# Kernel tuning notes

Hardware: AMD Instinct MI355X
Metric: run time of the kernel (lower is better)

## Reference

```python
import jax, jax.numpy as jnp
import numpy as np

B, N, S, D, H = 32, 16384, 8, 64, 128  # batch, num_inputs, num_slots, slot_size(==input_size), mlp_hidden
ITERS = 3
EPS = 1e-8
LN_EPS = 1e-5


def _ln(x, g, b):
    m = jnp.mean(x, axis=-1, keepdims=True)
    v = jnp.mean((x - m) ** 2, axis=-1, keepdims=True)
    return (x - m) * jax.lax.rsqrt(v + LN_EPS) * g + b


def setup_inputs() -> dict:
    key = jax.random.key(0)
    ks = jax.random.split(key, 20)
    s = 0.02
    return {
        "x": jax.random.normal(ks[0], (B, N, D), jnp.float32),
        "slot_noise": jax.random.normal(ks[1], (B, S, D), jnp.float32),
        "slots_mu": jax.random.normal(ks[2], (1, S, D), jnp.float32),
        "slots_log_sigma": jax.random.normal(ks[3], (1, S, D), jnp.float32) * 0.1,
        "ln_in_g": jnp.ones((D,), jnp.float32), "ln_in_b": jnp.zeros((D,), jnp.float32),
        "ln_slot_g": jnp.ones((D,), jnp.float32), "ln_slot_b": jnp.zeros((D,), jnp.float32),
        "ln_mlp_g": jnp.ones((D,), jnp.float32), "ln_mlp_b": jnp.zeros((D,), jnp.float32),
        "Wq": jax.random.normal(ks[4], (D, D), jnp.float32) * s,
        "Wk": jax.random.normal(ks[5], (D, D), jnp.float32) * s,
        "Wv": jax.random.normal(ks[6], (D, D), jnp.float32) * s,
        "W_ih": jax.random.normal(ks[7], (3 * D, D), jnp.float32) * s,
        "W_hh": jax.random.normal(ks[8], (3 * D, D), jnp.float32) * s,
        "b_ih": jnp.zeros((3 * D,), jnp.float32),
        "b_hh": jnp.zeros((3 * D,), jnp.float32),
        "W1": jax.random.normal(ks[9], (H, D), jnp.float32) * s,
        "b1": jnp.zeros((H,), jnp.float32),
        "W2": jax.random.normal(ks[10], (D, H), jnp.float32) * s,
        "b2": jnp.zeros((D,), jnp.float32),
    }


def reference(x, slot_noise, slots_mu, slots_log_sigma,
              ln_in_g, ln_in_b, ln_slot_g, ln_slot_b, ln_mlp_g, ln_mlp_b,
              Wq, Wk, Wv, W_ih, W_hh, b_ih, b_hh, W1, b1, W2, b2):
    inputs = _ln(x, ln_in_g, ln_in_b)                      # [B,N,D]
    keys = inputs @ Wk.T                                   # [B,N,D]
    values = inputs @ Wv.T                                 # [B,N,D]
    slots = slots_mu + jnp.exp(slots_log_sigma) * slot_noise  # [B,S,D]
    scale = D ** (-0.5)
    for _ in range(ITERS):
        slots_prev = slots
        q = (_ln(slots, ln_slot_g, ln_slot_b) @ Wq.T) * scale   # [B,S,D]
        attn = jax.nn.softmax(jnp.einsum('bnd,bsd->bns', keys, q), axis=2) + EPS
        attn = attn / jnp.sum(attn, axis=1, keepdims=True)      # weighted mean over inputs
        updates = jnp.einsum('bns,bnd->bsd', attn, values)      # [B,S,D]
        # GRUCell(update, hidden=slots_prev), torch semantics
        gi = updates @ W_ih.T + b_ih
        gh = slots_prev @ W_hh.T + b_hh
        i_r, i_z, i_n = jnp.split(gi, 3, axis=-1)
        h_r, h_z, h_n = jnp.split(gh, 3, axis=-1)
        r = jax.nn.sigmoid(i_r + h_r)
        z = jax.nn.sigmoid(i_z + h_z)
        n = jnp.tanh(i_n + r * h_n)
        upd = (1.0 - z) * n + z * slots_prev
        # residual MLP (full_skip=False: residual around updates)
        slots = upd + jax.nn.relu(_ln(upd, ln_mlp_g, ln_mlp_b) @ W1.T + b1) @ W2.T + b2
    return slots
```

## Files before the change

kernel.cpp:

```cpp
#include <hip/hip_runtime.h>

#define BB 32
#define NN 16384

typedef __attribute__((ext_vector_type(4))) float f4;
typedef __attribute__((ext_vector_type(8))) short short8;

__device__ __forceinline__ unsigned int f2bf(float f) {
  unsigned int u = __float_as_uint(f);
  return (u + 0x7fffu + ((u >> 16) & 1u)) >> 16;
}
__device__ __forceinline__ short bfs(float f) { return (short)f2bf(f); }

__device__ __forceinline__ unsigned int pk4_fp8(float a, float b, float c, float d) {
  int w = __builtin_amdgcn_cvt_pk_fp8_f32(a, b, 0, false);
  w = __builtin_amdgcn_cvt_pk_fp8_f32(c, d, w, true);
  return (unsigned int)w;
}

__global__ void __launch_bounds__(256) prep_kernel(
    const float* __restrict__ Wq, const float* __restrict__ Wk,
    const float* __restrict__ W_ih, const float* __restrict__ Wv,
    float* __restrict__ M, float* __restrict__ Wihv)
{
  int id = blockIdx.x * 256 + threadIdx.x;
  if (id < 4096) {
    int e1 = id >> 6, e2 = id & 63;
    float acc = 0.f;
    for (int d = 0; d < 64; ++d) acc += Wq[d * 64 + e1] * Wk[d * 64 + e2];
    M[id] = acc;
  } else {
    int t = (id - 4096) >> 6, e = id & 63;
    float acc = 0.f;
    for (int k = 0; k < 64; ++k) acc += W_ih[t * 64 + k] * Wv[k * 64 + e];
    Wihv[t * 64 + e] = acc;
  }
}

__global__ void __launch_bounds__(64) init_qk_kernel(
    const float* __restrict__ noise, const float* __restrict__ mu,
    const float* __restrict__ lsig, float* __restrict__ slots,
    const float* __restrict__ gs, const float* __restrict__ bsl,
    const float* __restrict__ M, unsigned short* __restrict__ qkb16)
{
  const int bsi = blockIdx.x, l = threadIdx.x;
  const int idx = bsi * 64 + l;
  __shared__ float sh[64];
  float v = mu[idx & 511] + __expf(lsig[idx & 511]) * noise[idx];
  slots[idx] = v;
  float sm = v, sq = v * v;
#pragma unroll
  for (int m = 1; m < 64; m <<= 1) { sm += __shfl_xor(sm, m); sq += __shfl_xor(sq, m); }
  float mean = sm * (1.f / 64.f);
  float var = sq * (1.f / 64.f) - mean * mean;
  sh[l] = (v - mean) * rsqrtf(var + 1e-5f) * gs[l] + bsl[l];
  float acc = 0.f;
  for (int k = 0; k < 64; ++k) acc += sh[k] * M[k * 64 + l];
  qkb16[idx] = (unsigned short)f2bf(acc * 0.125f);
}

template <int MODE>
__global__ void __launch_bounds__(256) attn_kernel(
    const float* __restrict__ x, const unsigned char* __restrict__ Xin,
    const float* __restrict__ gin, const float* __restrict__ bin,
    unsigned char* __restrict__ Xout, unsigned char* __restrict__ XnT,
    const unsigned short* __restrict__ qkb16, const unsigned char* __restrict__ qkb8,
    float* __restrict__ Wpart, float* __restrict__ cpart)
{
  constexpr int SMS = (MODE == 0) ? 16896 : 5440;
  __shared__ __align__(16) unsigned short SMEM[SMS];

  const int tid = threadIdx.x, wave = tid >> 6, lane = tid & 63;
  const int l15 = lane & 15, quad = lane >> 4;
  const int blk = blockIdx.x;
  const int b = blk >> 5;
  const int k0 = quad * 8;

  unsigned short* xt  = (MODE == 0) ? (SMEM + wave * 3584) : nullptr;
  unsigned short* Pt16 = (MODE == 0) ? (SMEM + 14336 + wave * 640) : nullptr;
  unsigned char*  Pt8  = (MODE == 1) ? ((unsigned char*)SMEM + wave * 640) : nullptr;

  short8 qkA0_16, qkA1_16;
  unsigned long qkA0_8 = 0, qkA1_8 = 0;
  if constexpr (MODE == 0) {
    const unsigned short* qrow = qkb16 + (((b << 3) + (l15 & 7)) << 6) + k0;
    qkA0_16 = *(const short8*)qrow;
    qkA1_16 = *(const short8*)(qrow + 32);
  } else {
    const unsigned char* qrow = qkb8 + (((b << 3) + (l15 & 7)) << 6) + k0;
    qkA0_8 = *(const unsigned long*)qrow;
    qkA1_8 = *(const unsigned long*)(qrow + 32);
  }

  f4 g0a, g0b, g1a, g1b, h0a, h0b, h1a, h1b;
  if constexpr (MODE == 0) {
    g0a = *(const f4*)(gin + k0);      g0b = *(const f4*)(gin + k0 + 4);
    g1a = *(const f4*)(gin + k0 + 32); g1b = *(const f4*)(gin + k0 + 36);
    h0a = *(const f4*)(bin + k0);      h0b = *(const f4*)(bin + k0 + 4);
    h1a = *(const f4*)(bin + k0 + 32); h1b = *(const f4*)(bin + k0 + 36);
  }

  const size_t row00 = (size_t)blk * 512 + wave * 32 + l15;
  const int nt0 = ((blk & 31) << 4) + wave;

  f4 wacc[4];
#pragma unroll
  for (int t = 0; t < 4; ++t) wacc[t] = (f4){0.f, 0.f, 0.f, 0.f};
  float cac0 = 0.f, cac1 = 0.f, cac2 = 0.f, cac3 = 0.f;

  f4 cc[2][4];
  unsigned long a8[2][2];
  unsigned long cv[4];
  const unsigned char* vB =
      (MODE == 1) ? (XnT + ((((size_t)(b << 9)) + nt0) << 11) + (l15 << 5) + (quad << 3))
                  : nullptr;

  if constexpr (MODE == 0) {
    const float* xp = x + row00 * 64 + k0;
#pragma unroll
    for (int s = 0; s < 2; ++s) {
      const float* sp = xp + s * 1024;
      cc[s][0] = *(const f4*)sp;        cc[s][1] = *(const f4*)(sp + 4);
      cc[s][2] = *(const f4*)(sp + 32); cc[s][3] = *(const f4*)(sp + 36);
    }
  } else {
    const unsigned char* xb = Xin + row00 * 64 + k0;
#pragma unroll
    for (int s = 0; s < 2; ++s) {
      a8[s][0] = *(const unsigned long*)(xb + s * 1024);
      a8[s][1] = *(const unsigned long*)(xb + s * 1024 + 32);
    }
#pragma unroll
    for (int t = 0; t < 4; ++t)
      cv[t] = *(const unsigned long*)(vB + (t << 9));
  }

#pragma unroll
  for (int u = 0; u < 4; ++u) {
    f4 nc[2][4];
    unsigned long na[2][2], nv[4];
    if (u < 3) {
      if constexpr (MODE == 0) {
        const float* xp = x + (row00 + (size_t)(u + 1) * 128) * 64 + k0;
#pragma unroll
        for (int s = 0; s < 2; ++s) {
          const float* sp = xp + s * 1024;
          nc[s][0] = *(const f4*)sp;        nc[s][1] = *(const f4*)(sp + 4);
          nc[s][2] = *(const f4*)(sp + 32); nc[s][3] = *(const f4*)(sp + 36);
        }
      } else {
        const unsigned char* xb = Xin + (row00 + (size_t)(u + 1) * 128) * 64 + k0;
#pragma unroll
        for (int s = 0; s < 2; ++s) {
          na[s][0] = *(const unsigned long*)(xb + s * 1024);
          na[s][1] = *(const unsigned long*)(xb + s * 1024 + 32);
        }
#pragma unroll
        for (int t = 0; t < 4; ++t)
          nv[t] = *(const unsigned long*)(vB + (t << 9) + ((size_t)(u + 1) << 13));
      }
    }

#pragma unroll
    for (int s = 0; s < 2; ++s) {
      short8 a0_16, a1_16;
      f4 lg = (f4){0.f, 0.f, 0.f, 0.f};
      if constexpr (MODE == 0) {
        float sm = 0.f, sq = 0.f;
#pragma unroll
        for (int j = 0; j < 4; ++j) {
          float v0 = cc[s][0][j], v1 = cc[s][1][j], v2 = cc[s][2][j], v3 = cc[s][3][j];
          sm += v0 + v1 + v2 + v3;
          sq += v0 * v0 + v1 * v1 + v2 * v2 + v3 * v3;
        }
        sm += __shfl_xor(sm, 16); sq += __shfl_xor(sq, 16);
        sm += __shfl_xor(sm, 32); sq += __shfl_xor(sq, 32);
        const float mean = sm * (1.f / 64.f);
        const float var = sq * (1.f / 64.f) - mean * mean;
        const float rstd = rsqrtf(var + 1e-5f);
        float f0[8], f1[8];
#pragma unroll
        for (int j = 0; j < 4; ++j) {
          f0[j]     = (cc[s][0][j] - mean) * rstd * g0a[j] + h0a[j];
          f0[j + 4] = (cc[s][1][j] - mean) * rstd * g0b[j] + h0b[j];
          f1[j]     = (cc[s][2][j] - mean) * rstd * g1a[j] + h1a[j];
          f1[j + 4] = (cc[s][3][j] - mean) * rstd * g1b[j] + h1b[j];
        }
#pragma unroll
        for (int j = 0; j < 8; ++j) { a0_16[j] = bfs(f0[j]); a1_16[j] = bfs(f1[j]); }
        unsigned char* xo = Xout + (row00 + (size_t)u * 128 + s * 16) * 64 + k0;
        uint2 p0v2; p0v2.x = pk4_fp8(f0[0], f0[1], f0[2], f0[3]);
        p0v2.y = pk4_fp8(f0[4], f0[5], f0[6], f0[7]);
        *(uint2*)xo = p0v2;
        uint2 p1v2; p1v2.x = pk4_fp8(f1[0], f1[1], f1[2], f1[3]);
        p1v2.y = pk4_fp8(f1[4], f1[5], f1[6], f1[7]);
        *(uint2*)(xo + 32) = p1v2;
        const int nn = s * 16 + l15;
        unsigned short* xb0 = xt + (quad << 3) + nn;
#pragma unroll
        for (int jj = 0; jj < 8; ++jj) {
          xb0[(k0 + jj) * 56]      = (unsigned short)a0_16[jj];
          xb0[(k0 + jj + 32) * 56] = (unsigned short)a1_16[jj];
        }
        lg = __builtin_amdgcn_mfma_f32_16x16x32_bf16(qkA0_16, a0_16, lg, 0, 0, 0);
        lg = __builtin_amdgcn_mfma_f32_16x16x32_bf16(qkA1_16, a1_16, lg, 0, 0, 0);
      } else {
        lg = __builtin_amdgcn_mfma_f32_16x16x32_fp8_fp8(
            (long)qkA0_8, (long)a8[s][0], lg, 0, 0, 0);
        lg = __builtin_amdgcn_mfma_f32_16x16x32_fp8_fp8(
            (long)qkA1_8, (long)a8[s][1], lg, 0, 0, 0);
      }

      const float e0 = __expf(lg[0]), e1 = __expf(lg[1]);
      const float e2 = __expf(lg[2]), e3 = __expf(lg[3]);
      float ss = e0 + e1 + e2 + e3;
      ss += __shfl_xor(ss, 16);
      ss += __shfl_xor(ss, 32);
      const float rs = __builtin_amdgcn_rcpf(ss * 0.5f);
      const float p0 = e0 * rs, p1 = e1 * rs, p2 = e2 * rs, p3 = e3 * rs;
      cac0 += p0; cac1 += p1; cac2 += p2; cac3 += p3;
      if constexpr (MODE == 0) {
        unsigned short* pw = Pt16 + (quad << 2) * 40 + s * 16 + l15;
        pw[0]   = (unsigned short)f2bf(p0);
        pw[40]  = (unsigned short)f2bf(p1);
        pw[80]  = (unsigned short)f2bf(p2);
        pw[120] = (unsigned short)f2bf(p3);
      } else {
        unsigned char* pw = Pt8 + (quad << 2) * 40 + s * 16 + l15;
        const unsigned int w1 = (unsigned int)__builtin_amdgcn_cvt_pk_fp8_f32(p0, p1, 0, false);
        const unsigned int w2 = (unsigned int)__builtin_amdgcn_cvt_pk_fp8_f32(p2, p3, 0, false);
        pw[0]   = (unsigned char)(w1 & 0xff);
        pw[40]  = (unsigned char)((w1 >> 8) & 0xff);
        pw[80]  = (unsigned char)(w2 & 0xff);
        pw[120] = (unsigned char)((w2 >> 8) & 0xff);
      }
    }

    if constexpr (MODE == 0) {
      short8 pf = *(const short8*)(Pt16 + l15 * 40 + quad * 8);
#pragma unroll
      for (int t = 0; t < 4; ++t) {
        const int rr = t * 16 + l15;
        const short8 cvv =
            *(const short8*)(xt + rr * 56 + (((rr >> 3) & 3) << 3) + (quad << 3));
        wacc[t] = __builtin_amdgcn_mfma_f32_16x16x32_bf16(pf, cvv, wacc[t], 0, 0, 0);
      }
      unsigned char* tb = XnT + ((((size_t)(b << 9)) + nt0 + (u << 2)) << 11);
#pragma unroll
      for (int pass = 0; pass < 4; ++pass) {
        const int e = (pass << 4) + (lane >> 2);
        const int no = (lane & 3) << 3;
        const short8 vv =
            *(const short8*)(xt + e * 56 + (((e >> 3) & 3) << 3) + no);
        float g[8];
#pragma unroll
        for (int j = 0; j < 8; ++j)
          g[j] = __uint_as_float(((unsigned int)(unsigned short)vv[j]) << 16);
        uint2 ov; ov.x = pk4_fp8(g[0], g[1], g[2], g[3]);
        ov.y = pk4_fp8(g[4], g[5], g[6], g[7]);
        *(uint2*)(tb + (e << 5) + no) = ov;
      }
    } else {
      const unsigned long pf = *(const unsigned long*)(Pt8 + l15 * 40 + quad * 8);
#pragma unroll
      for (int t = 0; t < 4; ++t)
        wacc[t] = __builtin_amdgcn_mfma_f32_16x16x32_fp8_fp8(
            (long)pf, (long)cv[t], wacc[t], 0, 0, 0);
    }

    if (u < 3) {
      if constexpr (MODE == 0) {
#pragma unroll
        for (int s = 0; s < 2; ++s)
#pragma unroll
          for (int j = 0; j < 4; ++j) cc[s][j] = nc[s][j];
      } else {
#pragma unroll
        for (int s = 0; s < 2; ++s) { a8[s][0] = na[s][0]; a8[s][1] = na[s][1]; }
#pragma unroll
        for (int t = 0; t < 4; ++t) cv[t] = nv[t];
      }
    }
  }

#pragma unroll
  for (int m = 1; m < 16; m <<= 1) {
    cac0 += __shfl_xor(cac0, m); cac1 += __shfl_xor(cac1, m);
    cac2 += __shfl_xor(cac2, m); cac3 += __shfl_xor(cac3, m);
  }
  float* redw;
  float* credw;
  if constexpr (MODE == 0) {
    redw  = (float*)(SMEM + wave * 3584);
    credw = (float*)(SMEM + wave * 3584 + 1024);
  } else {
    redw  = (float*)(SMEM + 1280) + wave * 512;
    credw = (float*)(SMEM + 5376) + wave * 8;
  }
  if (l15 == 0 && quad < 2) {
    credw[quad * 4 + 0] = cac0; credw[quad * 4 + 1] = cac1;
    credw[quad * 4 + 2] = cac2; credw[quad * 4 + 3] = cac3;
  }
  if (quad < 2) {
#pragma unroll
    for (int t = 0; t < 4; ++t)
#pragma unroll
      for (int r = 0; r < 4; ++r)
        redw[(quad * 4 + r) * 64 + (t << 4) + l15] = wacc[t][r];
  }
  __syncthreads();
  for (int i = tid; i < 512; i += 256) {
    float acc = 0.f;
#pragma unroll
    for (int w = 0; w < 4; ++w) {
      const float* rw = (MODE == 0) ? (const float*)(SMEM + w * 3584)
                                    : (const float*)(SMEM + 1280) + w * 512;
      acc += rw[i];
    }
    Wpart[(size_t)blk * 512 + i] = acc;
  }
  if (tid < 8) {
    float acc = 0.f;
#pragma unroll
    for (int w = 0; w < 4; ++w) {
      const float* cw = (MODE == 0) ? (const float*)(SMEM + w * 3584 + 1024)
                                    : (const float*)(SMEM + 5376) + w * 8;
      acc += cw[tid];
    }
    cpart[blk * 8 + tid] = acc;
  }
}

__global__ void __launch_bounds__(256) update_kernel(
    const float* __restrict__ Wpart, const float* __restrict__ cpart,
    const float* __restrict__ slots, float* __restrict__ out,
    const float* __restrict__ Wihv, const float* __restrict__ W_hh,
    const float* __restrict__ b_ih, const float* __restrict__ b_hh,
    const float* __restrict__ g_mlp, const float* __restrict__ b_mlp,
    const float* __restrict__ W1, const float* __restrict__ b1,
    const float* __restrict__ W2, const float* __restrict__ b2,
    const float* __restrict__ gs, const float* __restrict__ bsl,
    const float* __restrict__ M, unsigned char* __restrict__ qkb8, int make_q)
{
  const int bs = blockIdx.x;
  const int b = bs >> 3, s = bs & 7;
  const int tid = threadIdx.x;
  const int l = tid & 63, cq = tid >> 6;
  __shared__ float wred[4][64];
  __shared__ float credS[4];
  __shared__ float u_sh[64], sp_sh[64], giA[192], ghA[192], uln_sh[64], h_sh[128];

  float wp = 0.f, cp2 = 0.f;
  for (int c = cq * 8; c < cq * 8 + 8; ++c) {
    wp += Wpart[(size_t)(((b << 5) + c) * 8 + s) * 64 + l];
    cp2 += cpart[((b << 5) + c) * 8 + s];
  }
  wred[cq][l] = wp;
  if (l == 0) credS[cq] = cp2;
  __syncthreads();

  float sp = 0.f;
  if (tid < 64) {
    const float cs = credS[0] + credS[1] + credS[2] + credS[3];
    const float u = (wred[0][l] + wred[1][l] + wred[2][l] + wred[3][l]) / cs;
    sp = slots[(b * 8 + s) * 64 + l];
    u_sh[l] = u; sp_sh[l] = sp;
  }
  __syncthreads();

  if (tid < 192) {
    float accI = b_ih[tid], accH = b_hh[tid];
    const float* wi = Wihv + tid * 64;
    const float* wh = W_hh + tid * 64;
    for (int k = 0; k < 64; ++k) { accI += u_sh[k] * wi[k]; accH += sp_sh[k] * wh[k]; }
    giA[tid] = accI; ghA[tid] = accH;
  }
  __syncthreads();

  float upd = 0.f;
  if (tid < 64) {
    const float rg = 1.f / (1.f + __expf(-(giA[l] + ghA[l])));
    const float zg = 1.f / (1.f + __expf(-(giA[64 + l] + ghA[64 + l])));
    const float ng = tanhf(giA[128 + l] + rg * ghA[128 + l]);
    upd = (1.f - zg) * ng + zg * sp;
    float sm = upd, sq = upd * upd;
#pragma unroll
    for (int m = 1; m < 64; m <<= 1) { sm += __shfl_xor(sm, m); sq += __shfl_xor(sq, m); }
    const float mean = sm * (1.f / 64.f);
    const float var = sq * (1.f / 64.f) - mean * mean;
    uln_sh[l] = (upd - mean) * rsqrtf(var + 1e-5f) * g_mlp[l] + b_mlp[l];
  }
  __syncthreads();

  if (tid < 128) {
    float acc = b1[tid];
    const float* w1 = W1 + tid * 64;
    for (int k = 0; k < 64; ++k) acc += uln_sh[k] * w1[k];
    h_sh[tid] = fmaxf(acc, 0.f);
  }
  __syncthreads();

  if (tid < 64) {
    float acc = b2[l];
    const float* w2 = W2 + l * 128;
    for (int k = 0; k < 128; ++k) acc += h_sh[k] * w2[k];
    const float sv = upd + acc;
    out[(b * 8 + s) * 64 + l] = sv;
    if (make_q) {
      float sm2 = sv, sq2 = sv * sv;
#pragma unroll
      for (int m = 1; m < 64; m <<= 1) { sm2 += __shfl_xor(sm2, m); sq2 += __shfl_xor(sq2, m); }
      const float mean2 = sm2 * (1.f / 64.f);
      const float var2 = sq2 * (1.f / 64.f) - mean2 * mean2;
      u_sh[l] = (sv - mean2) * rsqrtf(var2 + 1e-5f) * gs[l] + bsl[l];
      float qa = 0.f;
      for (int k = 0; k < 64; ++k) qa += u_sh[k] * M[k * 64 + l];
      const unsigned int w =
          (unsigned int)__builtin_amdgcn_cvt_pk_fp8_f32(qa * 0.125f, 0.f, 0, false);
      qkb8[(b * 8 + s) * 64 + l] = (unsigned char)(w & 0xff);
    }
  }
}

extern "C" void kernel_launch(void* const* d_in, const int* in_sizes, int n_in,
                              void* d_out, int out_size, void* d_ws, size_t ws_size,
                              hipStream_t stream) {
  const float* x       = (const float*)d_in[0];
  const float* noise   = (const float*)d_in[1];
  const float* mu      = (const float*)d_in[2];
  const float* lsig    = (const float*)d_in[3];
  const float* ln_in_g = (const float*)d_in[4];
  const float* ln_in_b = (const float*)d_in[5];
  const float* ln_sl_g = (const float*)d_in[6];
  const float* ln_sl_b = (const float*)d_in[7];
  const float* ln_ml_g = (const float*)d_in[8];
  const float* ln_ml_b = (const float*)d_in[9];
  const float* Wq      = (const float*)d_in[10];
  const float* Wk      = (const float*)d_in[11];
  const float* Wv      = (const float*)d_in[12];
  const float* W_ih    = (const float*)d_in[13];
  const float* W_hh    = (const float*)d_in[14];
  const float* b_ih    = (const float*)d_in[15];
  const float* b_hh    = (const float*)d_in[16];
  const float* W1      = (const float*)d_in[17];
  const float* b1      = (const float*)d_in[18];
  const float* W2      = (const float*)d_in[19];
  const float* b2      = (const float*)d_in[20];

  unsigned char* Xn8   = (unsigned char*)d_ws;
  unsigned char* XnT8  = Xn8 + (size_t)BB * NN * 64;
  unsigned short* qk16 = (unsigned short*)(XnT8 + (size_t)BB * NN * 64);
  unsigned char* qk8   = (unsigned char*)(qk16 + 16384);
  float* M     = (float*)(qk8 + 16384);
  float* Wihv  = M + 4096;
  float* slots = Wihv + 12288;
  float* Wpart = slots + 16384;
  float* cpart = Wpart + (size_t)1024 * 512;

  prep_kernel<<<dim3(64), dim3(256), 0, stream>>>(Wq, Wk, W_ih, Wv, M, Wihv);
  init_qk_kernel<<<dim3(256), dim3(64), 0, stream>>>(
      noise, mu, lsig, slots, ln_sl_g, ln_sl_b, M, qk16);

  attn_kernel<0><<<dim3(1024), dim3(256), 0, stream>>>(
      x, nullptr, ln_in_g, ln_in_b, Xn8, XnT8, qk16, nullptr, Wpart, cpart);

  for (int it = 0; it < 3; ++it) {
    update_kernel<<<dim3(256), dim3(256), 0, stream>>>(
        Wpart, cpart, slots, (it == 2) ? (float*)d_out : slots,
        Wihv, W_hh, b_ih, b_hh, ln_ml_g, ln_ml_b, W1, b1, W2, b2,
        ln_sl_g, ln_sl_b, M, qk8, (it < 2) ? 1 : 0);
    if (it < 2)
      attn_kernel<1><<<dim3(1024), dim3(256), 0, stream>>>(
          x, Xn8, ln_in_g, ln_in_b, nullptr, XnT8, nullptr, qk8, Wpart, cpart);
  }
}
```

Before: 298.5 us.

## Halve attention block work, split grid to 2048 blocks, restructure fp8 mode loads

The first attention pass now runs 128-thread blocks over 256 rows each, with half the shared memory and launch bounds set for more resident blocks. The fp8 pass keeps 256 threads but each block covers 256 rows in two unrolled steps, and all loads are issued up front instead of through a rolling prefetch. The update kernel now reduces 64 partials per batch instead of 32. This aims to raise occupancy and parallelism, at the cost of more partial-sum traffic and more reduction work.

```diff
diff --git a/kernel.cpp b/kernel.cpp
--- a/kernel.cpp
+++ b/kernel.cpp
@@ -60,24 +60,25 @@
 }
 
 template <int MODE>
-__global__ void __launch_bounds__(256) attn_kernel(
+__global__ void __launch_bounds__(MODE == 0 ? 128 : 256, MODE == 0 ? 5 : 6)
+attn_kernel(
     const float* __restrict__ x, const unsigned char* __restrict__ Xin,
     const float* __restrict__ gin, const float* __restrict__ bin,
     unsigned char* __restrict__ Xout, unsigned char* __restrict__ XnT,
     const unsigned short* __restrict__ qkb16, const unsigned char* __restrict__ qkb8,
     float* __restrict__ Wpart, float* __restrict__ cpart)
 {
-  constexpr int SMS = (MODE == 0) ? 16896 : 5440;
+  constexpr int SMS = (MODE == 0) ? 8448 : 5440;
   __shared__ __align__(16) unsigned short SMEM[SMS];
 
   const int tid = threadIdx.x, wave = tid >> 6, lane = tid & 63;
   const int l15 = lane & 15, quad = lane >> 4;
   const int blk = blockIdx.x;
-  const int b = blk >> 5;
+  const int b = blk >> 6;
   const int k0 = quad * 8;
 
-  unsigned short* xt  = (MODE == 0) ? (SMEM + wave * 3584) : nullptr;
-  unsigned short* Pt16 = (MODE == 0) ? (SMEM + 14336 + wave * 640) : nullptr;
+  unsigned short* xt   = (MODE == 0) ? (SMEM + wave * 3584) : nullptr;
+  unsigned short* Pt16 = (MODE == 0) ? (SMEM + 7168 + wave * 640) : nullptr;
   unsigned char*  Pt8  = (MODE == 1) ? ((unsigned char*)SMEM + wave * 640) : nullptr;
 
   short8 qkA0_16, qkA1_16;
@@ -100,72 +101,39 @@
     h1a = *(const f4*)(bin + k0 + 32); h1b = *(const f4*)(bin + k0 + 36);
   }
 
-  const size_t row00 = (size_t)blk * 512 + wave * 32 + l15;
-  const int nt0 = ((blk & 31) << 4) + wave;
+  const size_t row00 = (size_t)blk * 256 + wave * 32 + l15;
+  const int nt0 = ((blk & 63) << 3) + wave;
 
   f4 wacc[4];
 #pragma unroll
   for (int t = 0; t < 4; ++t) wacc[t] = (f4){0.f, 0.f, 0.f, 0.f};
   float cac0 = 0.f, cac1 = 0.f, cac2 = 0.f, cac3 = 0.f;
 
-  f4 cc[2][4];
-  unsigned long a8[2][2];
-  unsigned long cv[4];
-  const unsigned char* vB =
-      (MODE == 1) ? (XnT + ((((size_t)(b << 9)) + nt0) << 11) + (l15 << 5) + (quad << 3))
-                  : nullptr;
-
   if constexpr (MODE == 0) {
-    const float* xp = x + row00 * 64 + k0;
-#pragma unroll
-    for (int s = 0; s < 2; ++s) {
-      const float* sp = xp + s * 1024;
-      cc[s][0] = *(const f4*)sp;        cc[s][1] = *(const f4*)(sp + 4);
-      cc[s][2] = *(const f4*)(sp + 32); cc[s][3] = *(const f4*)(sp + 36);
-    }
-  } else {
-    const unsigned char* xb = Xin + row00 * 64 + k0;
-#pragma unroll
-    for (int s = 0; s < 2; ++s) {
-      a8[s][0] = *(const unsigned long*)(xb + s * 1024);
-      a8[s][1] = *(const unsigned long*)(xb + s * 1024 + 32);
-    }
-#pragma unroll
-    for (int t = 0; t < 4; ++t)
-      cv[t] = *(const unsigned long*)(vB + (t << 9));
-  }
-
-#pragma unroll
-  for (int u = 0; u < 4; ++u) {
-    f4 nc[2][4];
-    unsigned long na[2][2], nv[4];
-    if (u < 3) {
-      if constexpr (MODE == 0) {
-        const float* xp = x + (row00 + (size_t)(u + 1) * 128) * 64 + k0;
+    f4 cc[2][4];
+    {
+      const float* xp = x + row00 * 64 + k0;
+#pragma unroll
+      for (int s = 0; s < 2; ++s) {
+        const float* sp = xp + s * 1024;
+        cc[s][0] = *(const f4*)sp;        cc[s][1] = *(const f4*)(sp + 4);
+        cc[s][2] = *(const f4*)(sp + 32); cc[s][3] = *(const f4*)(sp + 36);
+      }
+    }
+#pragma unroll
+    for (int u = 0; u < 4; ++u) {
+      f4 nc[2][4];
+      if (u < 3) {
+        const float* xp = x + (row00 + (size_t)(u + 1) * 64) * 64 + k0;
 #pragma unroll
         for (int s = 0; s < 2; ++s) {
           const float* sp = xp + s * 1024;
           nc[s][0] = *(const f4*)sp;        nc[s][1] = *(const f4*)(sp + 4);
           nc[s][2] = *(const f4*)(sp + 32); nc[s][3] = *(const f4*)(sp + 36);
         }
-      } else {
-        const unsigned char* xb = Xin + (row00 + (size_t)(u + 1) * 128) * 64 + k0;
-#pragma unroll
-        for (int s = 0; s < 2; ++s) {
-          na[s][0] = *(const unsigned long*)(xb + s * 1024);
-          na[s][1] = *(const unsigned long*)(xb + s * 1024 + 32);
-        }
-#pragma unroll
-        for (int t = 0; t < 4; ++t)
-          nv[t] = *(const unsigned long*)(vB + (t << 9) + ((size_t)(u + 1) << 13));
-      }
-    }
-
-#pragma unroll
-    for (int s = 0; s < 2; ++s) {
-      short8 a0_16, a1_16;
-      f4 lg = (f4){0.f, 0.f, 0.f, 0.f};
-      if constexpr (MODE == 0) {
+      }
+#pragma unroll
+      for (int s = 0; s < 2; ++s) {
         float sm = 0.f, sq = 0.f;
 #pragma unroll
         for (int j = 0; j < 4; ++j) {
@@ -186,15 +154,16 @@
           f1[j]     = (cc[s][2][j] - mean) * rstd * g1a[j] + h1a[j];
           f1[j + 4] = (cc[s][3][j] - mean) * rstd * g1b[j] + h1b[j];
         }
+        short8 a0_16, a1_16;
 #pragma unroll
         for (int j = 0; j < 8; ++j) { a0_16[j] = bfs(f0[j]); a1_16[j] = bfs(f1[j]); }
-        unsigned char* xo = Xout + (row00 + (size_t)u * 128 + s * 16) * 64 + k0;
-        uint2 p0v2; p0v2.x = pk4_fp8(f0[0], f0[1], f0[2], f0[3]);
-        p0v2.y = pk4_fp8(f0[4], f0[5], f0[6], f0[7]);
-        *(uint2*)xo = p0v2;
-        uint2 p1v2; p1v2.x = pk4_fp8(f1[0], f1[1], f1[2], f1[3]);
-        p1v2.y = pk4_fp8(f1[4], f1[5], f1[6], f1[7]);
-        *(uint2*)(xo + 32) = p1v2;
+        unsigned char* xo = Xout + (row00 + (size_t)u * 64 + s * 16) * 64 + k0;
+        uint2 pv0; pv0.x = pk4_fp8(f0[0], f0[1], f0[2], f0[3]);
+        pv0.y = pk4_fp8(f0[4], f0[5], f0[6], f0[7]);
+        *(uint2*)xo = pv0;
+        uint2 pv1; pv1.x = pk4_fp8(f1[0], f1[1], f1[2], f1[3]);
+        pv1.y = pk4_fp8(f1[4], f1[5], f1[6], f1[7]);
+        *(uint2*)(xo + 32) = pv1;
         const int nn = s * 16 + l15;
         unsigned short* xb0 = xt + (quad << 3) + nn;
 #pragma unroll
@@ -202,30 +171,87 @@
           xb0[(k0 + jj) * 56]      = (unsigned short)a0_16[jj];
           xb0[(k0 + jj + 32) * 56] = (unsigned short)a1_16[jj];
         }
+        f4 lg = (f4){0.f, 0.f, 0.f, 0.f};
         lg = __builtin_amdgcn_mfma_f32_16x16x32_bf16(qkA0_16, a0_16, lg, 0, 0, 0);
         lg = __builtin_amdgcn_mfma_f32_16x16x32_bf16(qkA1_16, a1_16, lg, 0, 0, 0);
-      } else {
-        lg = __builtin_amdgcn_mfma_f32_16x16x32_fp8_fp8(
-            (long)qkA0_8, (long)a8[s][0], lg, 0, 0, 0);
-        lg = __builtin_amdgcn_mfma_f32_16x16x32_fp8_fp8(
-            (long)qkA1_8, (long)a8[s][1], lg, 0, 0, 0);
-      }
-
-      const float e0 = __expf(lg[0]), e1 = __expf(lg[1]);
-      const float e2 = __expf(lg[2]), e3 = __expf(lg[3]);
-      float ss = e0 + e1 + e2 + e3;
-      ss += __shfl_xor(ss, 16);
-      ss += __shfl_xor(ss, 32);
-      const float rs = __builtin_amdgcn_rcpf(ss * 0.5f);
-      const float p0 = e0 * rs, p1 = e1 * rs, p2 = e2 * rs, p3 = e3 * rs;
-      cac0 += p0; cac1 += p1; cac2 += p2; cac3 += p3;
-      if constexpr (MODE == 0) {
+        const float e0 = __expf(lg[0]), e1 = __expf(lg[1]);
+        const float e2 = __expf(lg[2]), e3 = __expf(lg[3]);
+        float ss = e0 + e1 + e2 + e3;
+        ss += __shfl_xor(ss, 16);
+        ss += __shfl_xor(ss, 32);
+        const float rs = __builtin_amdgcn_rcpf(ss * 0.5f);
+        const float p0 = e0 * rs, p1 = e1 * rs, p2 = e2 * rs, p3 = e3 * rs;
+        cac0 += p0; cac1 += p1; cac2 += p2; cac3 += p3;
         unsigned short* pw = Pt16 + (quad << 2) * 40 + s * 16 + l15;
         pw[0]   = (unsigned short)f2bf(p0);
         pw[40]  = (unsigned short)f2bf(p1);
         pw[80]  = (unsigned short)f2bf(p2);
         pw[120] = (unsigned short)f2bf(p3);
-      } else {
+      }
+      short8 pf = *(const short8*)(Pt16 + l15 * 40 + quad * 8);
+#pragma unroll
+      for (int t = 0; t < 4; ++t) {
+        const int rr = t * 16 + l15;
+        const short8 cvv =
+            *(const short8*)(xt + rr * 56 + (((rr >> 3) & 3) << 3) + (quad << 3));
+        wacc[t] = __builtin_amdgcn_mfma_f32_16x16x32_bf16(pf, cvv, wacc[t], 0, 0, 0);
+      }
+      unsigned char* tb = XnT + ((((size_t)(b << 9)) + nt0 + (u << 1)) << 11);
+#pragma unroll
+      for (int pass = 0; pass < 4; ++pass) {
+        const int e = (pass << 4) + (lane >> 2);
+        const int no = (lane & 3) << 3;
+        const short8 vv =
+            *(const short8*)(xt + e * 56 + (((e >> 3) & 3) << 3) + no);
+        float g[8];
+#pragma unroll
+        for (int j = 0; j < 8; ++j)
+          g[j] = __uint_as_float(((unsigned int)(unsigned short)vv[j]) << 16);
+        uint2 ov; ov.x = pk4_fp8(g[0], g[1], g[2], g[3]);
+        ov.y = pk4_fp8(g[4], g[5], g[6], g[7]);
+        *(uint2*)(tb + (e << 5) + no) = ov;
+      }
+      if (u < 3) {
+#pragma unroll
+        for (int s = 0; s < 2; ++s)
+#pragma unroll
+          for (int j = 0; j < 4; ++j) cc[s][j] = nc[s][j];
+      }
+    }
+  } else {
+    unsigned long a8[2][2][2];
+    unsigned long cv8[2][4];
+    const unsigned char* vB =
+        XnT + ((((size_t)(b << 9)) + nt0) << 11) + (l15 << 5) + (quad << 3);
+#pragma unroll
+    for (int u = 0; u < 2; ++u) {
+      const unsigned char* xb = Xin + (row00 + (size_t)u * 128) * 64 + k0;
+#pragma unroll
+      for (int s = 0; s < 2; ++s) {
+        a8[u][s][0] = *(const unsigned long*)(xb + s * 1024);
+        a8[u][s][1] = *(const unsigned long*)(xb + s * 1024 + 32);
+      }
+#pragma unroll
+      for (int t = 0; t < 4; ++t)
+        cv8[u][t] = *(const unsigned long*)(vB + (t << 9) + ((size_t)u << 13));
+    }
+#pragma unroll
+    for (int u = 0; u < 2; ++u) {
+#pragma unroll
+      for (int s = 0; s < 2; ++s) {
+        f4 lg = (f4){0.f, 0.f, 0.f, 0.f};
+        lg = __builtin_amdgcn_mfma_f32_16x16x32_fp8_fp8(
+            (long)qkA0_8, (long)a8[u][s][0], lg, 0, 0, 0);
+        lg = __builtin_amdgcn_mfma_f32_16x16x32_fp8_fp8(
+            (long)qkA1_8, (long)a8[u][s][1], lg, 0, 0, 0);
+        const float e0 = __expf(lg[0]), e1 = __expf(lg[1]);
+        const float e2 = __expf(lg[2]), e3 = __expf(lg[3]);
+        float ss = e0 + e1 + e2 + e3;
+        ss += __shfl_xor(ss, 16);
+        ss += __shfl_xor(ss, 32);
+        const float rs = __builtin_amdgcn_rcpf(ss * 0.5f);
+        const float p0 = e0 * rs, p1 = e1 * rs, p2 = e2 * rs, p3 = e3 * rs;
+        cac0 += p0; cac1 += p1; cac2 += p2; cac3 += p3;
         unsigned char* pw = Pt8 + (quad << 2) * 40 + s * 16 + l15;
         const unsigned int w1 = (unsigned int)__builtin_amdgcn_cvt_pk_fp8_f32(p0, p1, 0, false);
         const unsigned int w2 = (unsigned int)__builtin_amdgcn_cvt_pk_fp8_f32(p2, p3, 0, false);
@@ -234,52 +260,11 @@
         pw[80]  = (unsigned char)(w2 & 0xff);
         pw[120] = (unsigned char)((w2 >> 8) & 0xff);
       }
-    }
-
-    if constexpr (MODE == 0) {
-      short8 pf = *(const short8*)(Pt16 + l15 * 40 + quad * 8);
-#pragma unroll
-      for (int t = 0; t < 4; ++t) {
-        const int rr = t * 16 + l15;
-        const short8 cvv =
-            *(const short8*)(xt + rr * 56 + (((rr >> 3) & 3) << 3) + (quad << 3));
-        wacc[t] = __builtin_amdgcn_mfma_f32_16x16x32_bf16(pf, cvv, wacc[t], 0, 0, 0);
-      }
-      unsigned char* tb = XnT + ((((size_t)(b << 9)) + nt0 + (u << 2)) << 11);
-#pragma unroll
-      for (int pass = 0; pass < 4; ++pass) {
-        const int e = (pass << 4) + (lane >> 2);
-        const int no = (lane & 3) << 3;
-        const short8 vv =
-            *(const short8*)(xt + e * 56 + (((e >> 3) & 3) << 3) + no);
-        float g[8];
-#pragma unroll
-        for (int j = 0; j < 8; ++j)
-          g[j] = __uint_as_float(((unsigned int)(unsigned short)vv[j]) << 16);
-        uint2 ov; ov.x = pk4_fp8(g[0], g[1], g[2], g[3]);
-        ov.y = pk4_fp8(g[4], g[5], g[6], g[7]);
-        *(uint2*)(tb + (e << 5) + no) = ov;
-      }
-    } else {
       const unsigned long pf = *(const unsigned long*)(Pt8 + l15 * 40 + quad * 8);
 #pragma unroll
       for (int t = 0; t < 4; ++t)
         wacc[t] = __builtin_amdgcn_mfma_f32_16x16x32_fp8_fp8(
-            (long)pf, (long)cv[t], wacc[t], 0, 0, 0);
-    }
-
-    if (u < 3) {
-      if constexpr (MODE == 0) {
-#pragma unroll
-        for (int s = 0; s < 2; ++s)
-#pragma unroll
-          for (int j = 0; j < 4; ++j) cc[s][j] = nc[s][j];
-      } else {
-#pragma unroll
-        for (int s = 0; s < 2; ++s) { a8[s][0] = na[s][0]; a8[s][1] = na[s][1]; }
-#pragma unroll
-        for (int t = 0; t < 4; ++t) cv[t] = nv[t];
-      }
+            (long)pf, (long)cv8[u][t], wacc[t], 0, 0, 0);
     }
   }
 
@@ -309,10 +294,12 @@
         redw[(quad * 4 + r) * 64 + (t << 4) + l15] = wacc[t][r];
   }
   __syncthreads();
-  for (int i = tid; i < 512; i += 256) {
+  constexpr int NW = (MODE == 0) ? 2 : 4;
+  constexpr int BT = (MODE == 0) ? 128 : 256;
+  for (int i = tid; i < 512; i += BT) {
     float acc = 0.f;
 #pragma unroll
-    for (int w = 0; w < 4; ++w) {
+    for (int w = 0; w < NW; ++w) {
       const float* rw = (MODE == 0) ? (const float*)(SMEM + w * 3584)
                                     : (const float*)(SMEM + 1280) + w * 512;
       acc += rw[i];
@@ -322,7 +309,7 @@
   if (tid < 8) {
     float acc = 0.f;
 #pragma unroll
-    for (int w = 0; w < 4; ++w) {
+    for (int w = 0; w < NW; ++w) {
       const float* cw = (MODE == 0) ? (const float*)(SMEM + w * 3584 + 1024)
                                     : (const float*)(SMEM + 5376) + w * 8;
       acc += cw[tid];
@@ -351,9 +338,9 @@
   __shared__ float u_sh[64], sp_sh[64], giA[192], ghA[192], uln_sh[64], h_sh[128];
 
   float wp = 0.f, cp2 = 0.f;
-  for (int c = cq * 8; c < cq * 8 + 8; ++c) {
-    wp += Wpart[(size_t)(((b << 5) + c) * 8 + s) * 64 + l];
-    cp2 += cpart[((b << 5) + c) * 8 + s];
+  for (int c = cq * 16; c < cq * 16 + 16; ++c) {
+    wp += Wpart[(size_t)(((b << 6) + c) * 8 + s) * 64 + l];
+    cp2 += cpart[((b << 6) + c) * 8 + s];
   }
   wred[cq][l] = wp;
   if (l == 0) credS[cq] = cp2;
@@ -455,13 +442,13 @@
   float* Wihv  = M + 4096;
   float* slots = Wihv + 12288;
   float* Wpart = slots + 16384;
-  float* cpart = Wpart + (size_t)1024 * 512;
+  float* cpart = Wpart + (size_t)2048 * 512;
 
   prep_kernel<<<dim3(64), dim3(256), 0, stream>>>(Wq, Wk, W_ih, Wv, M, Wihv);
   init_qk_kernel<<<dim3(256), dim3(64), 0, stream>>>(
       noise, mu, lsig, slots, ln_sl_g, ln_sl_b, M, qk16);
 
-  attn_kernel<0><<<dim3(1024), dim3(256), 0, stream>>>(
+  attn_kernel<0><<<dim3(2048), dim3(128), 0, stream>>>(
       x, nullptr, ln_in_g, ln_in_b, Xn8, XnT8, qk16, nullptr, Wpart, cpart);
 
   for (int it = 0; it < 3; ++it) {
@@ -470,7 +457,7 @@
         Wihv, W_hh, b_ih, b_hh, ln_ml_g, ln_ml_b, W1, b1, W2, b2,
         ln_sl_g, ln_sl_b, M, qk8, (it < 2) ? 1 : 0);
     if (it < 2)
-      attn_kernel<1><<<dim3(1024), dim3(256), 0, stream>>>(
+      attn_kernel<1><<<dim3(2048), dim3(256), 0, stream>>>(
           x, Xn8, ln_in_g, ln_in_b, nullptr, XnT8, nullptr, qk8, Wpart, cpart);
   }
 }
```

Measured after the change: 457.6 us. 53.3% more time.
